# Performance work log

Measured on AMD Instinct MI355X. Metric: run time of the kernel, lower is better.

## Reference

```python
import jax, jax.numpy as jnp
import numpy as np

D_MODEL = 1024
NHEAD = 16
HEAD_DIM = D_MODEL // NHEAD
MASK_FILLER = -1e20


def setup_inputs() -> dict:
    key = jax.random.key(0)
    ks = jax.random.split(key, 8)
    B, S = 2, 2048
    query = jax.random.normal(ks[0], (B, S, D_MODEL), dtype=jnp.float32)
    key_t = jax.random.normal(ks[1], (B, S, D_MODEL), dtype=jnp.float32)
    value = jax.random.normal(ks[2], (B, S, D_MODEL), dtype=jnp.float32)
    mask = jax.random.randint(ks[3], (B, S, S), 0, 2, dtype=jnp.int32)
    # nn.Linear(d_model, d_model, bias=False) weights, shape [out, in]
    scale = 1.0 / np.sqrt(D_MODEL)
    wq = jax.random.uniform(ks[4], (D_MODEL, D_MODEL), jnp.float32, -scale, scale)
    wk = jax.random.uniform(ks[5], (D_MODEL, D_MODEL), jnp.float32, -scale, scale)
    wv = jax.random.uniform(ks[6], (D_MODEL, D_MODEL), jnp.float32, -scale, scale)
    wo = jax.random.uniform(ks[7], (D_MODEL, D_MODEL), jnp.float32, -scale, scale)
    return {"query": query, "key": key_t, "value": value, "mask": mask,
            "wq": wq, "wk": wk, "wv": wv, "wo": wo}


def reference(query, key, value, mask, wq, wk, wv, wo):
    B = query.shape[0]
    # Projections: nn.Linear -> x @ W.T
    q = (query @ wq.T).reshape(B, -1, NHEAD, HEAD_DIM).transpose(0, 2, 1, 3)  # [B,H,Sq,Dh]
    k = (key @ wk.T).reshape(B, -1, NHEAD, HEAD_DIM).transpose(0, 2, 1, 3)    # [B,H,Sk,Dh]
    v = (value @ wv.T).reshape(B, -1, NHEAD, HEAD_DIM).transpose(0, 2, 1, 3)  # [B,H,Sk,Dh]
    scores = jnp.einsum('bhqd,bhkd->bhqk', q, k) / jnp.sqrt(jnp.float32(HEAD_DIM))
    scores = jnp.where(mask[:, None, :, :] == 0, MASK_FILLER, scores)
    attn = jax.nn.softmax(scores, axis=-1)  # dropout p=0.0 -> identity
    out = jnp.einsum('bhqk,bhkd->bhqd', attn, v)  # [B,H,Sq,Dh]
    out = out.transpose(0, 2, 1, 3).reshape(B, -1, D_MODEL)
    return out @ wo.T
```

## Files before the change

kernel.cpp:

```cpp
#include <hip/hip_runtime.h>
#include <stdint.h>

typedef __bf16 bf16x8 __attribute__((ext_vector_type(8)));
typedef __bf16 bf16x4 __attribute__((ext_vector_type(4)));
typedef float floatx4 __attribute__((ext_vector_type(4)));
typedef unsigned short ushort8v __attribute__((ext_vector_type(8)));
typedef unsigned int uint4v __attribute__((ext_vector_type(4)));
typedef unsigned short u16;
typedef unsigned long long u64;

#define GLOAD_LDS16(gp, lp)                                                       \
  __builtin_amdgcn_global_load_lds((__attribute__((address_space(1))) void*)(gp), \
                                   (__attribute__((address_space(3))) void*)(lp), \
                                   16, 0, 0)

__device__ __forceinline__ u16 f2bf(float f) {
  uint32_t u = __builtin_bit_cast(uint32_t, f);
  u = (u + 0x7FFFu + ((u >> 16) & 1u)) >> 16;
  return (u16)u;
}

__device__ __forceinline__ ushort8v load8(const void* base, size_t elemOff, int isf32) {
  if (isf32) {
    const uint32_t* p = (const uint32_t*)base + elemOff;
    uint4v a = *(const uint4v*)p;
    uint4v b = *(const uint4v*)(p + 4);
#pragma unroll
    for (int i = 0; i < 4; ++i) { a[i] += 0x8000u; b[i] += 0x8000u; }
    uint4v r;
    r[0] = __builtin_amdgcn_perm(a[1], a[0], 0x07060302);
    r[1] = __builtin_amdgcn_perm(a[3], a[2], 0x07060302);
    r[2] = __builtin_amdgcn_perm(b[1], b[0], 0x07060302);
    r[3] = __builtin_amdgcn_perm(b[3], b[2], 0x07060302);
    return __builtin_bit_cast(ushort8v, r);
  }
  return *(const ushort8v*)((const u16*)base + elemOff);
}

__global__ void detect_dtype(const u16* __restrict__ q, int* __restrict__ flag) {
  if (threadIdx.x == 0) *flag = 0;
  __syncthreads();
  int hit = 0;
  for (int i = threadIdx.x; i < 8192; i += 256) {
    u16 u = q[i];
    if (((u >> 7) & 0xFF) == 0xFF) hit = 1;
  }
  if (hit) atomicOr(flag, 1);
}

__global__ __launch_bounds__(256)
void prep(const void* X0, const void* X1, const void* X2,
          const void* W0, const void* W1, const void* W2, const void* W3,
          u16* __restrict__ Xb, u16* __restrict__ Wb,
          const int* __restrict__ mask, u64* __restrict__ mpk,
          const int* __restrict__ flagp)
{
  const int id = blockIdx.x;
  const int t  = threadIdx.x;
  if (id < 8192) {
    const int isf = *flagp;
    const int r2  = t >> 7;
    const int col = (t & 127) * 8;
    const void* src; u16* dst; int row;
    if (id < 6144) {
      const int s = id >> 11;
      src = (s == 0) ? X0 : (s == 1) ? X1 : X2;
      row = (id & 2047) * 2 + r2;
      dst = Xb + (size_t)s * 4096 * 1040 + (size_t)row * 1040 + col;
    } else {
      const int s = (id - 6144) >> 9;
      src = (s == 0) ? W0 : (s == 1) ? W1 : (s == 2) ? W2 : W3;
      row = ((id - 6144) & 511) * 2 + r2;
      dst = Wb + (size_t)s * 1024 * 1040 + (size_t)row * 1040 + col;
    }
    *(ushort8v*)dst = load8(src, (size_t)row * 1024 + col, isf);
  } else {
    const int g    = (id - 8192) * 4 + (t >> 6);
    const int lane = t & 63;
#pragma unroll
    for (int i = 0; i < 4; ++i) {
      const int wordId = g * 4 + i;
      const int row  = wordId >> 5;
      const int word = wordId & 31;
      const int m = mask[(size_t)row * 2048 + word * 64 + lane];
      u64 bits = __ballot(m != 0);
      if (lane == 0) mpk[(size_t)row * 32 + word] = bits;
    }
  }
}

__global__ void pack_mask(const int* __restrict__ mask, u64* __restrict__ mpk) {
  const int gw   = (blockIdx.x * 256 + threadIdx.x) >> 6;
  const int lane = threadIdx.x & 63;
  const int word = gw & 31;
  const int row  = gw >> 5;
  const int m = mask[(size_t)row * 2048 + word * 64 + lane];
  u64 bits = __ballot(m != 0);
  if (lane == 0) mpk[(size_t)row * 32 + word] = bits;
}

__global__ __launch_bounds__(256)
void cvt_w(const void* W0, const void* W1, const void* W2, const void* W3,
           u16* __restrict__ dst, const int* __restrict__ flagp) {
  const int isf = *flagp;
  const int z = blockIdx.y;
  const void* src = (z == 0) ? W0 : (z == 1) ? W1 : (z == 2) ? W2 : W3;
  const size_t off = ((size_t)blockIdx.x * 256 + threadIdx.x) * 8;
  *(ushort8v*)(dst + (size_t)z * 1024 * 1024 + off) = load8(src, off, isf);
}

__global__ __launch_bounds__(256, 3)
void gemm_qkv_b(const u16* __restrict__ Xb, const u16* __restrict__ Wb,
                u16* __restrict__ Qb, u16* __restrict__ Kb, u16* __restrict__ Vt)
{
  const int AS = 1040, WS = 1040, N = 1024, K = 1024;
  const int z = blockIdx.z;
  const u16* A = Xb + (size_t)z * 4096 * AS;
  const u16* W = Wb + (size_t)z * 1024 * WS;

  __shared__ __align__(16) u16 lA[2 * 128 * 32];
  __shared__ __align__(16) u16 lB[2 * 128 * 32];

  const int tid  = threadIdx.x;
  const int lane = tid & 63;
  const int quad = lane >> 4;
  const int l15  = lane & 15;
  const int w    = tid >> 6;
  const int wm   = w >> 1, wn = w & 1;
  const int tileM = blockIdx.x * 128;
  const int tileN = blockIdx.y * 128;

  floatx4 acc[4][4] = {};

  const int ldRow = tid >> 2;
  const int ldCol = (tid & 3) * 8;
  const u16* aG = A + (size_t)(tileM + ldRow) * AS + ldCol;
  const u16* bG = W + (size_t)(tileN + ldRow) * WS + ldCol;
  u16* lAp = lA + tid * 8;
  u16* lBp = lB + tid * 8;

  GLOAD_LDS16(aG, lAp);
  GLOAD_LDS16(aG + (size_t)64 * AS, lAp + 2048);
  GLOAD_LDS16(bG, lBp);
  GLOAD_LDS16(bG + (size_t)64 * WS, lBp + 2048);
  __syncthreads();

#pragma unroll 2
  for (int k0 = 0; k0 < K; k0 += 32) {
    const int cur = (k0 >> 5) & 1;
    const int nxo = 4096 * (cur ^ 1);
    if (k0 + 32 < K) {
      GLOAD_LDS16(aG + k0 + 32, lAp + nxo);
      GLOAD_LDS16(aG + (size_t)64 * AS + k0 + 32, lAp + nxo + 2048);
      GLOAD_LDS16(bG + k0 + 32, lBp + nxo);
      GLOAD_LDS16(bG + (size_t)64 * WS + k0 + 32, lBp + nxo + 2048);
    }
    const u16* cA = lA + 4096 * cur;
    const u16* cB = lB + 4096 * cur;
    bf16x8 af[4], bw[4];
#pragma unroll
    for (int i = 0; i < 4; ++i) {
      af[i] = *(const bf16x8*)&cA[(wm * 64 + i * 16 + l15) * 32 + quad * 8];
      bw[i] = *(const bf16x8*)&cB[(wn * 64 + i * 16 + l15) * 32 + quad * 8];
    }
#pragma unroll
    for (int i = 0; i < 4; ++i)
#pragma unroll
      for (int j = 0; j < 4; ++j)
        acc[i][j] = __builtin_amdgcn_mfma_f32_16x16x32_bf16(af[i], bw[j], acc[i][j], 0, 0, 0);
    __syncthreads();
  }

  if (z < 2) {
    u16* C = (z == 0) ? Qb : Kb;
    const float sc = (z == 0) ? 0.18033688011112042f : 1.0f;
#pragma unroll
    for (int i = 0; i < 4; ++i) {
      const int row0 = tileM + wm * 64 + i * 16 + quad * 4;
#pragma unroll
      for (int j = 0; j < 4; ++j) {
        const int col = tileN + wn * 64 + j * 16 + l15;
#pragma unroll
        for (int r = 0; r < 4; ++r)
          C[(size_t)(row0 + r) * N + col] = f2bf(acc[i][j][r] * sc);
      }
    }
  } else {
    const int half = w >> 1;
    u16* myT = (w & 1) ? lB : lA;
#pragma unroll
    for (int pass = 0; pass < 2; ++pass) {
      __syncthreads();
      if (half == pass) {
#pragma unroll
        for (int i = 0; i < 4; ++i)
#pragma unroll
          for (int j = 0; j < 4; ++j)
#pragma unroll
            for (int r = 0; r < 4; ++r) {
              const int lr = i * 16 + quad * 4 + r;
              const int lc = j * 16 + l15;
              myT[lr * 64 + (lc ^ (quad << 4))] = f2bf(acc[i][j][r]);
            }
      }
      __syncthreads();
      if (half == pass) {
        const int n    = lane;
        const int gcol = tileN + wn * 64 + n;
        const int hh = gcol >> 6, dd = gcol & 63;
        const int growBase = tileM + wm * 64;
        const int bb = growBase >> 11;
        const int s0 = growBase & 2047;
        u16* dst = Vt + (((size_t)bb * 16 + hh) * 64 + dd) * 2048 + s0;
#pragma unroll
        for (int m0 = 0; m0 < 64; m0 += 8) {
          ushort8v pk;
#pragma unroll
          for (int t = 0; t < 8; ++t) {
            const int m = m0 + t;
            pk[t] = myT[m * 64 + (n ^ ((m & 12) << 2))];
          }
          *(ushort8v*)(dst + m0) = pk;
        }
      }
    }
  }
}

__global__ __launch_bounds__(256)
void gemm_qkv_f(const void* X0, const void* X1, const void* X2,
                const u16* __restrict__ Wb,
                u16* __restrict__ Qb, u16* __restrict__ Kb, u16* __restrict__ Vt,
                const int* __restrict__ flagp)
{
  const int K = 1024, N = 1024;
  const int isf = *flagp;
  const int z = blockIdx.z;
  const void* A_ = (z == 0) ? X0 : (z == 1) ? X1 : X2;
  const u16* W = Wb + (size_t)z * 1024 * 1024;

  __shared__ __align__(16) u16 lA[128 * 32];
  __shared__ __align__(16) u16 lB[128 * 32];

  const int tid  = threadIdx.x;
  const int lane = tid & 63;
  const int quad = lane >> 4;
  const int l15  = lane & 15;
  const int w    = tid >> 6;
  const int wm   = w >> 1, wn = w & 1;
  const int tileM = blockIdx.x * 128;
  const int tileN = blockIdx.y * 128;

  floatx4 acc[4][4] = {};

  const int ldRow = tid >> 2;
  const int ldCol = (tid & 3) * 8;
  const size_t aOff = (size_t)(tileM + ldRow) * K + ldCol;
  const u16* bG = W + (size_t)(tileN + ldRow) * K + ldCol;
  u16* lAp = lA + tid * 8;
  u16* lBp = lB + tid * 8;

  ushort8v a0 = load8(A_, aOff, isf);
  ushort8v a1 = load8(A_, aOff + (size_t)64 * K, isf);
  ushort8v b0 = *(const ushort8v*)bG;
  ushort8v b1 = *(const ushort8v*)(bG + (size_t)64 * K);

  for (int k0 = 0; k0 < K; k0 += 32) {
    __syncthreads();
    *(ushort8v*)lAp          = a0;
    *(ushort8v*)(lAp + 2048) = a1;
    *(ushort8v*)lBp          = b0;
    *(ushort8v*)(lBp + 2048) = b1;
    __syncthreads();

    if (k0 + 32 < K) {
      a0 = load8(A_, aOff + k0 + 32, isf);
      a1 = load8(A_, aOff + (size_t)64 * K + k0 + 32, isf);
      b0 = *(const ushort8v*)(bG + k0 + 32);
      b1 = *(const ushort8v*)(bG + (size_t)64 * K + k0 + 32);
    }

    bf16x8 af[4], bw[4];
#pragma unroll
    for (int i = 0; i < 4; ++i) {
      af[i] = *(const bf16x8*)&lA[(wm * 64 + i * 16 + l15) * 32 + quad * 8];
      bw[i] = *(const bf16x8*)&lB[(wn * 64 + i * 16 + l15) * 32 + quad * 8];
    }
#pragma unroll
    for (int i = 0; i < 4; ++i)
#pragma unroll
      for (int j = 0; j < 4; ++j)
        acc[i][j] = __builtin_amdgcn_mfma_f32_16x16x32_bf16(af[i], bw[j], acc[i][j], 0, 0, 0);
  }

  if (z < 2) {
    u16* C = (z == 0) ? Qb : Kb;
    const float sc = (z == 0) ? 0.18033688011112042f : 1.0f;
#pragma unroll
    for (int i = 0; i < 4; ++i) {
      const int row0 = tileM + wm * 64 + i * 16 + quad * 4;
#pragma unroll
      for (int j = 0; j < 4; ++j) {
        const int col = tileN + wn * 64 + j * 16 + l15;
#pragma unroll
        for (int r = 0; r < 4; ++r)
          C[(size_t)(row0 + r) * N + col] = f2bf(acc[i][j][r] * sc);
      }
    }
  } else {
    const int half = w >> 1;
    u16* myT = (w & 1) ? lB : lA;
#pragma unroll
    for (int pass = 0; pass < 2; ++pass) {
      __syncthreads();
      if (half == pass) {
#pragma unroll
        for (int i = 0; i < 4; ++i)
#pragma unroll
          for (int j = 0; j < 4; ++j)
#pragma unroll
            for (int r = 0; r < 4; ++r) {
              const int lr = i * 16 + quad * 4 + r;
              const int lc = j * 16 + l15;
              myT[lr * 64 + (lc ^ (quad << 4))] = f2bf(acc[i][j][r]);
            }
      }
      __syncthreads();
      if (half == pass) {
        const int n    = lane;
        const int gcol = tileN + wn * 64 + n;
        const int hh = gcol >> 6, dd = gcol & 63;
        const int growBase = tileM + wm * 64;
        const int bb = growBase >> 11;
        const int s0 = growBase & 2047;
        u16* dst = Vt + (((size_t)bb * 16 + hh) * 64 + dd) * 2048 + s0;
#pragma unroll
        for (int m0 = 0; m0 < 64; m0 += 8) {
          ushort8v pk;
#pragma unroll
          for (int t = 0; t < 8; ++t) {
            const int m = m0 + t;
            pk[t] = myT[m * 64 + (n ^ ((m & 12) << 2))];
          }
          *(ushort8v*)(dst + m0) = pk;
        }
      }
    }
  }
}

__global__ __launch_bounds__(256)
void attn(const u16* Qb, const u16* __restrict__ Kb, const u16* __restrict__ Vt,
          const u64* __restrict__ mpk, u16* AO, int aoStr)
{
  __shared__ __align__(16) u16 lK[2][64 * 64];
  __shared__ __align__(16) u16 lV[64 * 64];
  __shared__ __align__(16) u16 lP[4][32 * 64];

  const int tid  = threadIdx.x;
  const int lane = tid & 63;
  const int quad = lane >> 4;
  const int l15  = lane & 15;
  const int w    = tid >> 6;

  const int bh = blockIdx.x;
  const int qt = blockIdx.y;
  const int b  = bh >> 4;
  const int h  = bh & 15;
  const size_t rowB   = (size_t)b * 2048;
  const size_t vtBase = ((size_t)bh * 64) * 2048;
  const int qbase = qt * 128 + w * 32;

  bf16x8 aq[2][2];
#pragma unroll
  for (int g = 0; g < 2; ++g) {
    const u16* qp = Qb + (rowB + qbase + g * 16 + l15) * 1024 + h * 64 + quad * 8;
    aq[g][0] = *(const bf16x8*)qp;
    aq[g][1] = *(const bf16x8*)(qp + 32);
  }

  const ushort8v one_u = {0x3F80, 0x3F80, 0x3F80, 0x3F80, 0x3F80, 0x3F80, 0x3F80, 0x3F80};
  const bf16x8 ones = __builtin_bit_cast(bf16x8, one_u);

  floatx4 o[2][4];
  floatx4 l4[2];
#pragma unroll
  for (int g = 0; g < 2; ++g) {
    l4[g] = (floatx4){0.f, 0.f, 0.f, 0.f};
#pragma unroll
    for (int nb = 0; nb < 4; ++nb) o[g][nb] = (floatx4){0.f, 0.f, 0.f, 0.f};
  }

  const u64* mrow0 = mpk + (rowB + qbase + l15) * 32;
  const u64* mrow1 = mpk + (rowB + qbase + 16 + l15) * 32;
  u16* lPw = &lP[w][0];

  const int r1 = tid >> 3;
  const int cs = ((tid & 7) ^ (r1 & 7)) * 8;
  const u16* kSrc = Kb + (rowB + r1) * 1024 + h * 64 + cs;
  const u16* vSrc = Vt + vtBase + (size_t)r1 * 2048 + cs;

  GLOAD_LDS16(kSrc,                     &lK[0][tid * 8]);
  GLOAD_LDS16(kSrc + (size_t)32 * 1024, &lK[0][tid * 8 + 2048]);

#pragma unroll 2
  for (int kt = 0; kt < 32; ++kt) {
    const int cur = kt & 1;
    __syncthreads();

    {
      const u16* vS = vSrc + kt * 64;
      GLOAD_LDS16(vS,                     &lV[tid * 8]);
      GLOAD_LDS16(vS + (size_t)32 * 2048, &lV[tid * 8 + 2048]);
    }
    if (kt < 31) {
      const u16* kS = kSrc + (size_t)(kt + 1) * 64 * 1024;
      GLOAD_LDS16(kS,                     &lK[cur ^ 1][tid * 8]);
      GLOAD_LDS16(kS + (size_t)32 * 1024, &lK[cur ^ 1][tid * 8 + 2048]);
    }

    const u64 mw0 = mrow0[kt];
    const u64 mw1 = mrow1[kt];

#pragma unroll
    for (int nb = 0; nb < 4; ++nb) {
      const int row = nb * 16 + l15;
      const int swk = (row & 7) << 3;
      bf16x8 ak0 = *(const bf16x8*)&lK[cur][row * 64 + ((quad * 8) ^ swk)];
      bf16x8 ak1 = *(const bf16x8*)&lK[cur][row * 64 + ((quad * 8 + 32) ^ swk)];
      floatx4 s0 = {0.f, 0.f, 0.f, 0.f};
      floatx4 s1 = {0.f, 0.f, 0.f, 0.f};
      s0 = __builtin_amdgcn_mfma_f32_16x16x32_bf16(ak0, aq[0][0], s0, 0, 0, 0);
      s1 = __builtin_amdgcn_mfma_f32_16x16x32_bf16(ak0, aq[1][0], s1, 0, 0, 0);
      s0 = __builtin_amdgcn_mfma_f32_16x16x32_bf16(ak1, aq[0][1], s0, 0, 0, 0);
      s1 = __builtin_amdgcn_mfma_f32_16x16x32_bf16(ak1, aq[1][1], s1, 0, 0, 0);
      const int kb = nb * 16 + quad * 4;
      const uint32_t nib0 = (uint32_t)(mw0 >> kb) & 0xFu;
      const uint32_t nib1 = (uint32_t)(mw1 >> kb) & 0xFu;
      const float a0 = (nib0 & 1u) ? __builtin_amdgcn_exp2f(s0[0]) : 0.0f;
      const float a1 = (nib0 & 2u) ? __builtin_amdgcn_exp2f(s0[1]) : 0.0f;
      const float a2 = (nib0 & 4u) ? __builtin_amdgcn_exp2f(s0[2]) : 0.0f;
      const float a3 = (nib0 & 8u) ? __builtin_amdgcn_exp2f(s0[3]) : 0.0f;
      const float c0 = (nib1 & 1u) ? __builtin_amdgcn_exp2f(s1[0]) : 0.0f;
      const float c1 = (nib1 & 2u) ? __builtin_amdgcn_exp2f(s1[1]) : 0.0f;
      const float c2 = (nib1 & 4u) ? __builtin_amdgcn_exp2f(s1[2]) : 0.0f;
      const float c3 = (nib1 & 8u) ? __builtin_amdgcn_exp2f(s1[3]) : 0.0f;
      bf16x4 p0, p1;
      p0[0] = (__bf16)a0; p0[1] = (__bf16)a1;
      p0[2] = (__bf16)a2; p0[3] = (__bf16)a3;
      p1[0] = (__bf16)c0; p1[1] = (__bf16)c1;
      p1[2] = (__bf16)c2; p1[3] = (__bf16)c3;
      const int col = kb ^ ((l15 & 7) << 3);
      *(bf16x4*)&lPw[l15 * 64 + col]        = p0;
      *(bf16x4*)&lPw[(16 + l15) * 64 + col] = p1;
    }
    __syncthreads();

#pragma unroll
    for (int ks = 0; ks < 2; ++ks) {
      const int pc = (ks * 32 + quad * 8) ^ ((l15 & 7) << 3);
      bf16x8 ap0 = *(const bf16x8*)&lPw[l15 * 64 + pc];
      bf16x8 ap1 = *(const bf16x8*)&lPw[(16 + l15) * 64 + pc];
#pragma unroll
      for (int nb = 0; nb < 4; ++nb) {
        const int row = nb * 16 + l15;
        bf16x8 bv = *(const bf16x8*)&lV[row * 64 + ((ks * 32 + quad * 8) ^ ((row & 7) << 3))];
        o[0][nb] = __builtin_amdgcn_mfma_f32_16x16x32_bf16(ap0, bv, o[0][nb], 0, 0, 0);
        o[1][nb] = __builtin_amdgcn_mfma_f32_16x16x32_bf16(ap1, bv, o[1][nb], 0, 0, 0);
      }
      l4[0] = __builtin_amdgcn_mfma_f32_16x16x32_bf16(ap0, ones, l4[0], 0, 0, 0);
      l4[1] = __builtin_amdgcn_mfma_f32_16x16x32_bf16(ap1, ones, l4[1], 0, 0, 0);
    }
  }

#pragma unroll
  for (int g = 0; g < 2; ++g)
#pragma unroll
    for (int r = 0; r < 4; ++r) {
      const float inv = 1.0f / l4[g][r];
      const size_t orow = (rowB + qbase + g * 16 + quad * 4 + r) * aoStr + h * 64;
#pragma unroll
      for (int nb = 0; nb < 4; ++nb)
        AO[orow + nb * 16 + l15] = f2bf(o[g][nb][r] * inv);
    }
}

__global__ __launch_bounds__(256, 3)
void gemm_out(const u16* __restrict__ A, int aStr,
              const u16* __restrict__ W, int wStr, void* C_,
              const int* __restrict__ flagp)
{
  const int K = 1024, N = 1024;
  const int isf = *flagp;

  __shared__ __align__(16) u16 lA[2 * 64 * 32];
  __shared__ __align__(16) u16 lB[2 * 128 * 32];

  const int tid  = threadIdx.x;
  const int lane = tid & 63;
  const int quad = lane >> 4;
  const int l15  = lane & 15;
  const int w    = tid >> 6;
  const int tileM = blockIdx.x * 64;
  const int tileN = blockIdx.y * 128;

  floatx4 acc[4][2] = {};

  const int ldRow = tid >> 2;
  const int ldCol = (tid & 3) * 8;
  const u16* aG = A + (size_t)(tileM + ldRow) * aStr + ldCol;
  const u16* bG = W + (size_t)(tileN + ldRow) * wStr + ldCol;
  u16* lAp = lA + tid * 8;
  u16* lBp = lB + tid * 8;

  GLOAD_LDS16(aG, lAp);
  GLOAD_LDS16(bG, lBp);
  GLOAD_LDS16(bG + (size_t)64 * wStr, lBp + 2048);
  __syncthreads();

#pragma unroll 2
  for (int k0 = 0; k0 < K; k0 += 32) {
    const int cur = (k0 >> 5) & 1;
    const int nxA = 2048 * (cur ^ 1);
    const int nxB = 4096 * (cur ^ 1);
    if (k0 + 32 < K) {
      GLOAD_LDS16(aG + k0 + 32, lAp + nxA);
      GLOAD_LDS16(bG + k0 + 32, lBp + nxB);
      GLOAD_LDS16(bG + (size_t)64 * wStr + k0 + 32, lBp + nxB + 2048);
    }
    const u16* cA = lA + 2048 * cur;
    const u16* cB = lB + 4096 * cur;
    bf16x8 af[4], bw[2];
#pragma unroll
    for (int i = 0; i < 4; ++i)
      af[i] = *(const bf16x8*)&cA[(i * 16 + l15) * 32 + quad * 8];
#pragma unroll
    for (int j = 0; j < 2; ++j)
      bw[j] = *(const bf16x8*)&cB[(w * 32 + j * 16 + l15) * 32 + quad * 8];
#pragma unroll
    for (int i = 0; i < 4; ++i)
#pragma unroll
      for (int j = 0; j < 2; ++j)
        acc[i][j] = __builtin_amdgcn_mfma_f32_16x16x32_bf16(af[i], bw[j], acc[i][j], 0, 0, 0);
    __syncthreads();
  }

#pragma unroll
  for (int i = 0; i < 4; ++i) {
    const int row0 = tileM + i * 16 + quad * 4;
#pragma unroll
    for (int j = 0; j < 2; ++j) {
      const int col = tileN + w * 32 + j * 16 + l15;
#pragma unroll
      for (int r = 0; r < 4; ++r) {
        const size_t off = (size_t)(row0 + r) * N + col;
        if (isf) ((float*)C_)[off] = acc[i][j][r];
        else     ((u16*)C_)[off]   = f2bf(acc[i][j][r]);
      }
    }
  }
}

extern "C" void kernel_launch(void* const* d_in, const int* in_sizes, int n_in,
                              void* d_out, int out_size, void* d_ws, size_t ws_size,
                              hipStream_t stream)
{
  const int* mk = (const int*)d_in[3];

  int* flag = (int*)d_ws;
  u64* mpk  = (u64*)((char*)d_ws + 256);
  const size_t SZ = (size_t)4096 * 1024;
  u16* Qb = (u16*)((char*)d_ws + 256 + (size_t)1048576);
  u16* Kb = Qb + SZ;
  u16* Vt = Kb + SZ;
  u16* Wb = Vt + SZ;

  const size_t WB_PAD = (size_t)4 * 1024 * 1040;
  const size_t XB_PAD = (size_t)3 * 4096 * 1040;
  const size_t NEED = 256 + 1048576 + 3 * SZ * 2 + WB_PAD * 2 + XB_PAD * 2;

  detect_dtype<<<1, 256, 0, stream>>>((const u16*)d_in[0], flag);

  if (ws_size >= NEED) {
    u16* Xb = Wb + WB_PAD;
    prep<<<16384, 256, 0, stream>>>(d_in[0], d_in[1], d_in[2],
                                    d_in[4], d_in[5], d_in[6], d_in[7],
                                    Xb, Wb, mk, mpk, flag);
    gemm_qkv_b<<<dim3(32, 8, 3), 256, 0, stream>>>(Xb, Wb, Qb, Kb, Vt);
    u16* AOp = Xb;
    attn<<<dim3(32, 16), 256, 0, stream>>>(Qb, Kb, Vt, mpk, AOp, 1040);
    gemm_out<<<dim3(64, 8), 256, 0, stream>>>(AOp, 1040,
                                              Wb + (size_t)3 * 1024 * 1040, 1040,
                                              d_out, flag);
  } else {
    pack_mask<<<32768, 256, 0, stream>>>(mk, mpk);
    cvt_w<<<dim3(512, 4), 256, 0, stream>>>(d_in[4], d_in[5], d_in[6], d_in[7], Wb, flag);
    gemm_qkv_f<<<dim3(32, 8, 3), 256, 0, stream>>>(d_in[0], d_in[1], d_in[2],
                                                   Wb, Qb, Kb, Vt, flag);
    attn<<<dim3(32, 16), 256, 0, stream>>>(Qb, Kb, Vt, mpk, Qb, 1024);
    gemm_out<<<dim3(64, 8), 256, 0, stream>>>(Qb, 1024,
                                              Wb + (size_t)3 * 1024 * 1024, 1024,
                                              d_out, flag);
  }
}
```

Before: 272.1 us.

## Double-buffer V tiles in attention and shrink output GEMM tile to 64x64

The attention kernel now double-buffers the V tile in LDS, prefetching the next K and V tiles together one iteration ahead. It also drops the barrier between writing P and running the PV MFMAs, since each wave reads only its own P slab. This hides V load latency and removes a block-wide sync per key tile, at the cost of an extra 8 KB of LDS. Separately, the output projection GEMM uses 64x64 tiles with 1024 blocks and a higher occupancy hint, which trades per-block data reuse for more parallelism.

Result: no change. 273.7 us (+0.6%).

```diff
diff --git a/kernel.cpp b/kernel.cpp
--- a/kernel.cpp
+++ b/kernel.cpp
@@ -354,7 +354,7 @@
           const u64* __restrict__ mpk, u16* AO, int aoStr)
 {
   __shared__ __align__(16) u16 lK[2][64 * 64];
-  __shared__ __align__(16) u16 lV[64 * 64];
+  __shared__ __align__(16) u16 lV[2][64 * 64];
   __shared__ __align__(16) u16 lP[4][32 * 64];
 
   const int tid  = threadIdx.x;
@@ -402,21 +402,20 @@
 
   GLOAD_LDS16(kSrc,                     &lK[0][tid * 8]);
   GLOAD_LDS16(kSrc + (size_t)32 * 1024, &lK[0][tid * 8 + 2048]);
+  GLOAD_LDS16(vSrc,                     &lV[0][tid * 8]);
+  GLOAD_LDS16(vSrc + (size_t)32 * 2048, &lV[0][tid * 8 + 2048]);
 
 #pragma unroll 2
   for (int kt = 0; kt < 32; ++kt) {
     const int cur = kt & 1;
     __syncthreads();
-
-    {
-      const u16* vS = vSrc + kt * 64;
-      GLOAD_LDS16(vS,                     &lV[tid * 8]);
-      GLOAD_LDS16(vS + (size_t)32 * 2048, &lV[tid * 8 + 2048]);
-    }
     if (kt < 31) {
       const u16* kS = kSrc + (size_t)(kt + 1) * 64 * 1024;
+      const u16* vS = vSrc + (kt + 1) * 64;
       GLOAD_LDS16(kS,                     &lK[cur ^ 1][tid * 8]);
       GLOAD_LDS16(kS + (size_t)32 * 1024, &lK[cur ^ 1][tid * 8 + 2048]);
+      GLOAD_LDS16(vS,                     &lV[cur ^ 1][tid * 8]);
+      GLOAD_LDS16(vS + (size_t)32 * 2048, &lV[cur ^ 1][tid * 8 + 2048]);
     }
 
     const u64 mw0 = mrow0[kt];
@@ -454,7 +453,6 @@
       *(bf16x4*)&lPw[l15 * 64 + col]        = p0;
       *(bf16x4*)&lPw[(16 + l15) * 64 + col] = p1;
     }
-    __syncthreads();
 
 #pragma unroll
     for (int ks = 0; ks < 2; ++ks) {
@@ -464,7 +462,7 @@
 #pragma unroll
       for (int nb = 0; nb < 4; ++nb) {
         const int row = nb * 16 + l15;
-        bf16x8 bv = *(const bf16x8*)&lV[row * 64 + ((ks * 32 + quad * 8) ^ ((row & 7) << 3))];
+        bf16x8 bv = *(const bf16x8*)&lV[cur][row * 64 + ((ks * 32 + quad * 8) ^ ((row & 7) << 3))];
         o[0][nb] = __builtin_amdgcn_mfma_f32_16x16x32_bf16(ap0, bv, o[0][nb], 0, 0, 0);
         o[1][nb] = __builtin_amdgcn_mfma_f32_16x16x32_bf16(ap1, bv, o[1][nb], 0, 0, 0);
       }
@@ -485,7 +483,7 @@
     }
 }
 
-__global__ __launch_bounds__(256, 3)
+__global__ __launch_bounds__(256, 4)
 void gemm_out(const u16* __restrict__ A, int aStr,
               const u16* __restrict__ W, int wStr, void* C_,
               const int* __restrict__ flagp)
@@ -494,7 +492,7 @@
   const int isf = *flagp;
 
   __shared__ __align__(16) u16 lA[2 * 64 * 32];
-  __shared__ __align__(16) u16 lB[2 * 128 * 32];
+  __shared__ __align__(16) u16 lB[2 * 64 * 32];
 
   const int tid  = threadIdx.x;
   const int lane = tid & 63;
@@ -502,9 +500,9 @@
   const int l15  = lane & 15;
   const int w    = tid >> 6;
   const int tileM = blockIdx.x * 64;
-  const int tileN = blockIdx.y * 128;
-
-  floatx4 acc[4][2] = {};
+  const int tileN = blockIdx.y * 64;
+
+  floatx4 acc[4] = {};
 
   const int ldRow = tid >> 2;
   const int ldCol = (tid & 3) * 8;
@@ -515,48 +513,38 @@
 
   GLOAD_LDS16(aG, lAp);
   GLOAD_LDS16(bG, lBp);
-  GLOAD_LDS16(bG + (size_t)64 * wStr, lBp + 2048);
   __syncthreads();
 
 #pragma unroll 2
   for (int k0 = 0; k0 < K; k0 += 32) {
     const int cur = (k0 >> 5) & 1;
-    const int nxA = 2048 * (cur ^ 1);
-    const int nxB = 4096 * (cur ^ 1);
+    const int nx = 2048 * (cur ^ 1);
     if (k0 + 32 < K) {
-      GLOAD_LDS16(aG + k0 + 32, lAp + nxA);
-      GLOAD_LDS16(bG + k0 + 32, lBp + nxB);
-      GLOAD_LDS16(bG + (size_t)64 * wStr + k0 + 32, lBp + nxB + 2048);
+      GLOAD_LDS16(aG + k0 + 32, lAp + nx);
+      GLOAD_LDS16(bG + k0 + 32, lBp + nx);
     }
     const u16* cA = lA + 2048 * cur;
-    const u16* cB = lB + 4096 * cur;
-    bf16x8 af[4], bw[2];
+    const u16* cB = lB + 2048 * cur;
+    bf16x8 af[4], bw;
 #pragma unroll
     for (int i = 0; i < 4; ++i)
       af[i] = *(const bf16x8*)&cA[(i * 16 + l15) * 32 + quad * 8];
-#pragma unroll
-    for (int j = 0; j < 2; ++j)
-      bw[j] = *(const bf16x8*)&cB[(w * 32 + j * 16 + l15) * 32 + quad * 8];
+    bw = *(const bf16x8*)&cB[(w * 16 + l15) * 32 + quad * 8];
 #pragma unroll
     for (int i = 0; i < 4; ++i)
-#pragma unroll
-      for (int j = 0; j < 2; ++j)
-        acc[i][j] = __builtin_amdgcn_mfma_f32_16x16x32_bf16(af[i], bw[j], acc[i][j], 0, 0, 0);
+      acc[i] = __builtin_amdgcn_mfma_f32_16x16x32_bf16(af[i], bw, acc[i], 0, 0, 0);
     __syncthreads();
   }
 
 #pragma unroll
   for (int i = 0; i < 4; ++i) {
     const int row0 = tileM + i * 16 + quad * 4;
-#pragma unroll
-    for (int j = 0; j < 2; ++j) {
-      const int col = tileN + w * 32 + j * 16 + l15;
-#pragma unroll
-      for (int r = 0; r < 4; ++r) {
-        const size_t off = (size_t)(row0 + r) * N + col;
-        if (isf) ((float*)C_)[off] = acc[i][j][r];
-        else     ((u16*)C_)[off]   = f2bf(acc[i][j][r]);
-      }
+    const int col  = tileN + w * 16 + l15;
+#pragma unroll
+    for (int r = 0; r < 4; ++r) {
+      const size_t off = (size_t)(row0 + r) * N + col;
+      if (isf) ((float*)C_)[off] = acc[i][r];
+      else     ((u16*)C_)[off]   = f2bf(acc[i][r]);
     }
   }
 }
@@ -589,17 +577,17 @@
     gemm_qkv_b<<<dim3(32, 8, 3), 256, 0, stream>>>(Xb, Wb, Qb, Kb, Vt);
     u16* AOp = Xb;
     attn<<<dim3(32, 16), 256, 0, stream>>>(Qb, Kb, Vt, mpk, AOp, 1040);
-    gemm_out<<<dim3(64, 8), 256, 0, stream>>>(AOp, 1040,
-                                              Wb + (size_t)3 * 1024 * 1040, 1040,
-                                              d_out, flag);
+    gemm_out<<<dim3(64, 16), 256, 0, stream>>>(AOp, 1040,
+                                               Wb + (size_t)3 * 1024 * 1040, 1040,
+                                               d_out, flag);
   } else {
     pack_mask<<<32768, 256, 0, stream>>>(mk, mpk);
     cvt_w<<<dim3(512, 4), 256, 0, stream>>>(d_in[4], d_in[5], d_in[6], d_in[7], Wb, flag);
     gemm_qkv_f<<<dim3(32, 8, 3), 256, 0, stream>>>(d_in[0], d_in[1], d_in[2],
                                                    Wb, Qb, Kb, Vt, flag);
     attn<<<dim3(32, 16), 256, 0, stream>>>(Qb, Kb, Vt, mpk, Qb, 1024);
-    gemm_out<<<dim3(64, 8), 256, 0, stream>>>(Qb, 1024,
-                                              Wb + (size_t)3 * 1024 * 1024, 1024,
-                                              d_out, flag);
-  }
-}
+    gemm_out<<<dim3(64, 16), 256, 0, stream>>>(Qb, 1024,
+                                               Wb + (size_t)3 * 1024 * 1024, 1024,
+                                               d_out, flag);
+  }
+}
```
